# Kernel tuning notes

Measured on AMD Instinct MI355X. Metric: run time of the kernel, lower is better.

Reference implementation:

```python
import jax, jax.numpy as jnp
import numpy as np

B, L, C, D = 4, 128, 1024, 512

def setup_inputs() -> dict:
    key = jax.random.key(0)
    ks = jax.random.split(key, 6)
    scale = 1.0 / np.sqrt(D)
    return {
        "hidden": jax.random.normal(ks[0], (B, L, D), dtype=jnp.float32),
        "ctx": jax.random.normal(ks[1], (B, C, D), dtype=jnp.float32),
        "W": jax.random.normal(ks[2], (D, D), dtype=jnp.float32) * scale,
        "U": jax.random.normal(ks[3], (D, D), dtype=jnp.float32) * scale,
        "U_b": jax.random.normal(ks[4], (D,), dtype=jnp.float32) * scale,
        "V": jax.random.normal(ks[5], (D,), dtype=jnp.float32) * scale,
    }

def reference(hidden, ctx, W, U, U_b, V):
    # Bahdanau additive attention: softmax_j V . tanh(W h_i + U c_j + b)
    wq = jnp.einsum('bld,ed->ble', hidden, W)          # [B, L, D]
    uc = jnp.einsum('bcd,ed->bce', ctx, U) + U_b       # [B, C, D]
    s = jnp.tanh(wq[:, :, None, :] + uc[:, None, :, :])  # [B, L, C, D]
    align = jnp.einsum('blcd,d->blc', s, V)            # [B, L, C]
    return jax.nn.softmax(align, axis=-1)
```

## Files before the change

kernel.cpp:

```cpp
#include <hip/hip_runtime.h>
#include <hip/hip_bf16.h>


#define SCALE2 2.8853900817779268f
#define PART (4 * 128 * 1024)

typedef _Float16 f16x8 __attribute__((ext_vector_type(8)));
typedef float f32x4 __attribute__((ext_vector_type(4)));

__device__ __forceinline__ void gload16(const void* g, void* l) {
    __builtin_amdgcn_global_load_lds(
        (const __attribute__((address_space(1))) void*)g,
        (__attribute__((address_space(3))) void*)l,
        16, 0, 0);
}

__global__ __launch_bounds__(256) void gemm_mfma(
    const float* __restrict__ hidden, const float* __restrict__ ctx,
    const float* __restrict__ Wmat, const float* __restrict__ Umat,
    const float* __restrict__ U_b,
    float* __restrict__ ewq_t, float* __restrict__ euc_t)
{
    __shared__ __align__(16) _Float16 Xh[2][64][40];
    __shared__ __align__(16) _Float16 Xl[2][64][40];
    __shared__ __align__(16) _Float16 Wh[2][64][40];
    __shared__ __align__(16) _Float16 Wl[2][64][40];

    const int tid  = threadIdx.x;
    const int lane = tid & 63;
    const int w    = tid >> 6;

    const float *X, *Wm, *bias;
    float* Ct;
    int m0, crow0, Mb, bshift;
    {
        int gb = blockIdx.x;
        if (gb < 64) {
            m0 = (gb & 7) * 64; crow0 = (gb >> 3) * 64;
            X = hidden; Wm = Wmat; bias = nullptr; Ct = ewq_t; Mb = 128; bshift = 7;
        } else {
            int g = gb - 64;
            m0 = (g & 7) * 64; crow0 = (g >> 3) * 64;
            X = ctx; Wm = Umat; bias = U_b; Ct = euc_t; Mb = 1024; bshift = 10;
        }
    }

    const int sr = tid >> 2;
    const int sk = (tid & 3) * 8;
    const float* xsrc = X  + (size_t)(crow0 + sr) * 512 + sk;
    const float* wsrc = Wm + (size_t)(m0    + sr) * 512 + sk;

    f32x4 acc[4];
#pragma unroll
    for (int t = 0; t < 4; ++t) acc[t] = (f32x4){0.f, 0.f, 0.f, 0.f};

    float xr[8], wr[8];
    {
        float4 a = *(const float4*)(xsrc);
        float4 b = *(const float4*)(xsrc + 4);
        float4 c = *(const float4*)(wsrc);
        float4 d = *(const float4*)(wsrc + 4);
        xr[0]=a.x; xr[1]=a.y; xr[2]=a.z; xr[3]=a.w; xr[4]=b.x; xr[5]=b.y; xr[6]=b.z; xr[7]=b.w;
        wr[0]=c.x; wr[1]=c.y; wr[2]=c.z; wr[3]=c.w; wr[4]=d.x; wr[5]=d.y; wr[6]=d.z; wr[7]=d.w;
        f16x8 xh, xl, wh, wl;
#pragma unroll
        for (int i = 0; i < 8; ++i) {
            xh[i] = (_Float16)xr[i]; xl[i] = (_Float16)(xr[i] - (float)xh[i]);
            wh[i] = (_Float16)wr[i]; wl[i] = (_Float16)(wr[i] - (float)wh[i]);
        }
        *(f16x8*)&Xh[0][sr][sk] = xh; *(f16x8*)&Xl[0][sr][sk] = xl;
        *(f16x8*)&Wh[0][sr][sk] = wh; *(f16x8*)&Wl[0][sr][sk] = wl;
    }

    const int fr = lane & 15;
    const int fk = (lane >> 4) * 8;
    const int mrow = w * 16 + fr;

    for (int kc = 0; kc < 16; ++kc) {
        if (kc < 15) {
            float4 a = *(const float4*)(xsrc + (kc + 1) * 32);
            float4 b = *(const float4*)(xsrc + (kc + 1) * 32 + 4);
            float4 c = *(const float4*)(wsrc + (kc + 1) * 32);
            float4 d = *(const float4*)(wsrc + (kc + 1) * 32 + 4);
            xr[0]=a.x; xr[1]=a.y; xr[2]=a.z; xr[3]=a.w; xr[4]=b.x; xr[5]=b.y; xr[6]=b.z; xr[7]=b.w;
            wr[0]=c.x; wr[1]=c.y; wr[2]=c.z; wr[3]=c.w; wr[4]=d.x; wr[5]=d.y; wr[6]=d.z; wr[7]=d.w;
        }
        __syncthreads();
        const int bu = kc & 1;
        const f16x8 ah = *(const f16x8*)&Wh[bu][mrow][fk];
        const f16x8 al = *(const f16x8*)&Wl[bu][mrow][fk];
#pragma unroll
        for (int t = 0; t < 4; ++t) {
            const f16x8 bh = *(const f16x8*)&Xh[bu][t * 16 + fr][fk];
            const f16x8 bl = *(const f16x8*)&Xl[bu][t * 16 + fr][fk];
            acc[t] = __builtin_amdgcn_mfma_f32_16x16x32_f16(ah, bh, acc[t], 0, 0, 0);
            acc[t] = __builtin_amdgcn_mfma_f32_16x16x32_f16(ah, bl, acc[t], 0, 0, 0);
            acc[t] = __builtin_amdgcn_mfma_f32_16x16x32_f16(al, bh, acc[t], 0, 0, 0);
        }
        if (kc < 15) {
            f16x8 xh, xl, wh, wl;
#pragma unroll
            for (int i = 0; i < 8; ++i) {
                xh[i] = (_Float16)xr[i]; xl[i] = (_Float16)(xr[i] - (float)xh[i]);
                wh[i] = (_Float16)wr[i]; wl[i] = (_Float16)(wr[i] - (float)wh[i]);
            }
            *(f16x8*)&Xh[bu ^ 1][sr][sk] = xh; *(f16x8*)&Xl[bu ^ 1][sr][sk] = xl;
            *(f16x8*)&Wh[bu ^ 1][sr][sk] = wh; *(f16x8*)&Wl[bu ^ 1][sr][sk] = wl;
        }
    }

    const int rbase = m0 + w * 16 + (lane >> 4) * 4;
    float bl4[4] = {0.f, 0.f, 0.f, 0.f};
    if (bias) {
        float4 t = *(const float4*)&bias[rbase];
        bl4[0] = t.x; bl4[1] = t.y; bl4[2] = t.z; bl4[3] = t.w;
    }
    const int bidx = crow0 >> bshift;
    const int cl0  = crow0 & (Mb - 1);
    float* obase = Ct + ((size_t)bidx * 512 + rbase) * Mb + cl0 + fr;
#pragma unroll
    for (int r = 0; r < 4; ++r)
#pragma unroll
        for (int t = 0; t < 4; ++t)
            obase[(size_t)r * Mb + t * 16] =
                __builtin_amdgcn_exp2f(SCALE2 * (acc[t][r] + bl4[r]));
}

__global__ __launch_bounds__(256) void fused_align10(
    const float* __restrict__ ewq_t,
    const float* __restrict__ euc_t,
    const float* __restrict__ Vv,
    float* __restrict__ pout, float* __restrict__ pws)
{
    __shared__ __align__(16) float uc_s[2][16][256];
    __shared__ __align__(16) float wq_s[2][16][16];
    __shared__ float v_s[64];

    const int tid  = threadIdx.x;
    const int lane = tid & 63;
    const int w    = __builtin_amdgcn_readfirstlane(tid >> 6);
    const int c0   = blockIdx.x * 256;
    const int l0   = blockIdx.y * 16;
    const int z    = blockIdx.z;
    const int b    = z >> 3, h = z & 7;
    const int d0   = h * 64;

    const float* ucb = euc_t + ((size_t)b * 512 + d0) * 1024 + c0;
    const float* wqb = ewq_t + ((size_t)b * 512 + d0) * 128 + l0;

    if (tid < 64) v_s[tid] = Vv[d0 + tid];

#define STAGE(buf, chunk)                                                     \
    {                                                                         \
        _Pragma("unroll")                                                     \
        for (int i_ = 0; i_ < 4; ++i_) {                                      \
            const int d_ = w * 4 + i_;                                        \
            gload16(ucb + (size_t)((chunk) * 16 + d_) * 1024 + lane * 4,      \
                    &uc_s[buf][d_][0]);                                       \
        }                                                                     \
        if (w == 0)                                                           \
            gload16(wqb + (size_t)((chunk) * 16 + (lane >> 2)) * 128 +        \
                        (lane & 3) * 4,                                       \
                    &wq_s[buf][0][0]);                                        \
    }

    float acc[4][4];
#pragma unroll
    for (int i = 0; i < 4; ++i)
#pragma unroll
        for (int k = 0; k < 4; ++k) acc[i][k] = 0.0f;

#define COMPUTE(bu, ch)                                                       \
    do {                                                                      \
        float vr[16];                                                         \
        _Pragma("unroll")                                                     \
        for (int j_ = 0; j_ < 4; ++j_) {                                      \
            const float4 v4_ = *(const float4*)&v_s[(ch) * 16 + j_ * 4];      \
            vr[j_ * 4 + 0] = v4_.x; vr[j_ * 4 + 1] = v4_.y;                   \
            vr[j_ * 4 + 2] = v4_.z; vr[j_ * 4 + 3] = v4_.w;                   \
        }                                                                     \
        float nn[4][4], dn[4][4];                                             \
        {                                                                     \
            const float4 e = *(const float4*)&uc_s[bu][0][lane * 4];          \
            const float4 q = *(const float4*)&wq_s[bu][0][w * 4];             \
            const float ea[4] = {e.x, e.y, e.z, e.w};                         \
            const float qa[4] = {q.x, q.y, q.z, q.w};                         \
            _Pragma("unroll")                                                 \
            for (int i = 0; i < 4; ++i)                                       \
                _Pragma("unroll")                                             \
                for (int k = 0; k < 4; ++k) {                                 \
                    dn[i][k] = fmaf(qa[i], ea[k], 1.0f);                      \
                    nn[i][k] = vr[0];                                         \
                }                                                             \
        }                                                                     \
        _Pragma("unroll")                                                     \
        for (int dd = 1; dd < 16; ++dd) {                                     \
            const float4 e = *(const float4*)&uc_s[bu][dd][lane * 4];         \
            const float4 q = *(const float4*)&wq_s[bu][dd][w * 4];            \
            const float ea[4] = {e.x, e.y, e.z, e.w};                         \
            const float qa[4] = {q.x, q.y, q.z, q.w};                         \
            const float vv = vr[dd];                                          \
            _Pragma("unroll")                                                 \
            for (int i = 0; i < 4; ++i)                                       \
                _Pragma("unroll")                                             \
                for (int k = 0; k < 4; ++k) {                                 \
                    const float t_ = fmaf(qa[i], ea[k], 1.0f);                \
                    nn[i][k] = fmaf(nn[i][k], t_, vv * dn[i][k]);             \
                    dn[i][k] *= t_;                                           \
                }                                                             \
        }                                                                     \
        _Pragma("unroll")                                                     \
        for (int i = 0; i < 4; ++i)                                           \
            _Pragma("unroll")                                                 \
            for (int k = 0; k < 4; ++k)                                       \
                acc[i][k] = fmaf(nn[i][k],                                    \
                                 __builtin_amdgcn_rcpf(dn[i][k]), acc[i][k]); \
    } while (0)

    STAGE(0, 0);
    __syncthreads();

    for (int cc = 0; cc < 2; ++cc) {
        STAGE(1, 2 * cc + 1);
        COMPUTE(0, 2 * cc);
        __syncthreads();
        if (cc == 0) STAGE(0, 2);
        COMPUTE(1, 2 * cc + 1);
        __syncthreads();
    }
#undef STAGE
#undef COMPUTE

    float* pp = (h == 0) ? pout : pws + (size_t)(h - 1) * PART;
#pragma unroll
    for (int i = 0; i < 4; ++i) {
        float4 r;
        r.x = -2.0f * acc[i][0]; r.y = -2.0f * acc[i][1];
        r.z = -2.0f * acc[i][2]; r.w = -2.0f * acc[i][3];
        *(float4*)(pp + ((size_t)b * 128 + l0 + w * 4 + i) * 1024 + c0 + lane * 4) = r;
    }
}

__global__ __launch_bounds__(256) void softmax4(
    float* __restrict__ data, const float* __restrict__ pws)
{
    const int row  = blockIdx.x * 4 + (threadIdx.x >> 6);
    const int lane = threadIdx.x & 63;
    float* p = data + (size_t)row * 1024;

    float4 x[4];
#pragma unroll
    for (int j = 0; j < 4; ++j) x[j] = *(const float4*)(p + j * 256 + lane * 4);
#pragma unroll
    for (int t = 0; t < 7; ++t) {
        const float* q = pws + (size_t)t * PART + (size_t)row * 1024;
#pragma unroll
        for (int j = 0; j < 4; ++j) {
            const float4 a = *(const float4*)(q + j * 256 + lane * 4);
            x[j].x += a.x; x[j].y += a.y; x[j].z += a.z; x[j].w += a.w;
        }
    }

    float m = x[0].x;
#pragma unroll
    for (int j = 0; j < 4; ++j) {
        m = fmaxf(m, x[j].x); m = fmaxf(m, x[j].y);
        m = fmaxf(m, x[j].z); m = fmaxf(m, x[j].w);
    }
#pragma unroll
    for (int mask = 32; mask >= 1; mask >>= 1) m = fmaxf(m, __shfl_xor(m, mask, 64));

    const float LOG2E = 1.4426950408889634f;
    float s = 0.0f;
#pragma unroll
    for (int j = 0; j < 4; ++j) {
        x[j].x = __builtin_amdgcn_exp2f((x[j].x - m) * LOG2E);
        x[j].y = __builtin_amdgcn_exp2f((x[j].y - m) * LOG2E);
        x[j].z = __builtin_amdgcn_exp2f((x[j].z - m) * LOG2E);
        x[j].w = __builtin_amdgcn_exp2f((x[j].w - m) * LOG2E);
        s += x[j].x + x[j].y + x[j].z + x[j].w;
    }
#pragma unroll
    for (int mask = 32; mask >= 1; mask >>= 1) s += __shfl_xor(s, mask, 64);
    const float r = __builtin_amdgcn_rcpf(s);
#pragma unroll
    for (int j = 0; j < 4; ++j) {
        x[j].x *= r; x[j].y *= r; x[j].z *= r; x[j].w *= r;
        *(float4*)(p + j * 256 + lane * 4) = x[j];
    }
}

extern "C" void kernel_launch(void* const* d_in, const int* in_sizes, int n_in,
                              void* d_out, int out_size, void* d_ws, size_t ws_size,
                              hipStream_t stream)
{
    const float* hidden = (const float*)d_in[0];
    const float* ctx    = (const float*)d_in[1];
    const float* W      = (const float*)d_in[2];
    const float* U      = (const float*)d_in[3];
    const float* U_b    = (const float*)d_in[4];
    const float* V      = (const float*)d_in[5];
    float* out = (float*)d_out;

    float* ewq_t = (float*)d_ws;
    float* euc_t = ewq_t + 4 * 512 * 128;
    float* pws   = euc_t + 4 * 512 * 1024;

    gemm_mfma<<<576, 256, 0, stream>>>(hidden, ctx, W, U, U_b, ewq_t, euc_t);
    fused_align10<<<dim3(4, 8, 32), 256, 0, stream>>>(ewq_t, euc_t, V, out, pws);
    softmax4<<<128, 256, 0, stream>>>(out, pws);
}
```

Measured before the change: 51.81 us.

## Deepen GEMM prefetch, raise align priority, spread softmax one row per block

The GEMM kernel now keeps two register sets of raw fp32 data, so global loads are issued two K-chunks ahead and the loop is fully unrolled, which hides load latency better. The alignment kernel raises wave priority with s_setprio around its compute section to favour math issue over the staging waves. Softmax now uses one 256-thread block per row instead of one wave per row, giving 512 blocks for more parallelism, at the cost of LDS cross-wave reductions and two barriers. The deeper prefetch raises register pressure in the GEMM.

```diff
diff --git a/kernel.cpp b/kernel.cpp
--- a/kernel.cpp
+++ b/kernel.cpp
@@ -54,60 +54,74 @@
 #pragma unroll
     for (int t = 0; t < 4; ++t) acc[t] = (f32x4){0.f, 0.f, 0.f, 0.f};
 
-    float xr[8], wr[8];
-    {
-        float4 a = *(const float4*)(xsrc);
-        float4 b = *(const float4*)(xsrc + 4);
-        float4 c = *(const float4*)(wsrc);
-        float4 d = *(const float4*)(wsrc + 4);
-        xr[0]=a.x; xr[1]=a.y; xr[2]=a.z; xr[3]=a.w; xr[4]=b.x; xr[5]=b.y; xr[6]=b.z; xr[7]=b.w;
-        wr[0]=c.x; wr[1]=c.y; wr[2]=c.z; wr[3]=c.w; wr[4]=d.x; wr[5]=d.y; wr[6]=d.z; wr[7]=d.w;
-        f16x8 xh, xl, wh, wl;
-#pragma unroll
-        for (int i = 0; i < 8; ++i) {
-            xh[i] = (_Float16)xr[i]; xl[i] = (_Float16)(xr[i] - (float)xh[i]);
-            wh[i] = (_Float16)wr[i]; wl[i] = (_Float16)(wr[i] - (float)wh[i]);
-        }
-        *(f16x8*)&Xh[0][sr][sk] = xh; *(f16x8*)&Xl[0][sr][sk] = xl;
-        *(f16x8*)&Wh[0][sr][sk] = wh; *(f16x8*)&Wl[0][sr][sk] = wl;
+    float xrA[8], wrA[8], xrB[8], wrB[8];
+
+#define LOADRAW(xr_, wr_, chunk)                                              \
+    {                                                                         \
+        float4 a_ = *(const float4*)(xsrc + (chunk) * 32);                    \
+        float4 b_ = *(const float4*)(xsrc + (chunk) * 32 + 4);                \
+        float4 c_ = *(const float4*)(wsrc + (chunk) * 32);                    \
+        float4 d_ = *(const float4*)(wsrc + (chunk) * 32 + 4);                \
+        xr_[0]=a_.x; xr_[1]=a_.y; xr_[2]=a_.z; xr_[3]=a_.w;                   \
+        xr_[4]=b_.x; xr_[5]=b_.y; xr_[6]=b_.z; xr_[7]=b_.w;                   \
+        wr_[0]=c_.x; wr_[1]=c_.y; wr_[2]=c_.z; wr_[3]=c_.w;                   \
+        wr_[4]=d_.x; wr_[5]=d_.y; wr_[6]=d_.z; wr_[7]=d_.w;                   \
+    }
+
+#define CVTWRITE(xr_, wr_, buf)                                               \
+    {                                                                         \
+        f16x8 xh_, xl_, wh_, wl_;                                             \
+        _Pragma("unroll")                                                     \
+        for (int i_ = 0; i_ < 8; ++i_) {                                      \
+            xh_[i_] = (_Float16)xr_[i_];                                      \
+            xl_[i_] = (_Float16)(xr_[i_] - (float)xh_[i_]);                   \
+            wh_[i_] = (_Float16)wr_[i_];                                      \
+            wl_[i_] = (_Float16)(wr_[i_] - (float)wh_[i_]);                   \
+        }                                                                     \
+        *(f16x8*)&Xh[buf][sr][sk] = xh_; *(f16x8*)&Xl[buf][sr][sk] = xl_;     \
+        *(f16x8*)&Wh[buf][sr][sk] = wh_; *(f16x8*)&Wl[buf][sr][sk] = wl_;     \
     }
 
     const int fr = lane & 15;
     const int fk = (lane >> 4) * 8;
     const int mrow = w * 16 + fr;
 
-    for (int kc = 0; kc < 16; ++kc) {
-        if (kc < 15) {
-            float4 a = *(const float4*)(xsrc + (kc + 1) * 32);
-            float4 b = *(const float4*)(xsrc + (kc + 1) * 32 + 4);
-            float4 c = *(const float4*)(wsrc + (kc + 1) * 32);
-            float4 d = *(const float4*)(wsrc + (kc + 1) * 32 + 4);
-            xr[0]=a.x; xr[1]=a.y; xr[2]=a.z; xr[3]=a.w; xr[4]=b.x; xr[5]=b.y; xr[6]=b.z; xr[7]=b.w;
-            wr[0]=c.x; wr[1]=c.y; wr[2]=c.z; wr[3]=c.w; wr[4]=d.x; wr[5]=d.y; wr[6]=d.z; wr[7]=d.w;
-        }
-        __syncthreads();
-        const int bu = kc & 1;
-        const f16x8 ah = *(const f16x8*)&Wh[bu][mrow][fk];
-        const f16x8 al = *(const f16x8*)&Wl[bu][mrow][fk];
-#pragma unroll
-        for (int t = 0; t < 4; ++t) {
-            const f16x8 bh = *(const f16x8*)&Xh[bu][t * 16 + fr][fk];
-            const f16x8 bl = *(const f16x8*)&Xl[bu][t * 16 + fr][fk];
-            acc[t] = __builtin_amdgcn_mfma_f32_16x16x32_f16(ah, bh, acc[t], 0, 0, 0);
-            acc[t] = __builtin_amdgcn_mfma_f32_16x16x32_f16(ah, bl, acc[t], 0, 0, 0);
-            acc[t] = __builtin_amdgcn_mfma_f32_16x16x32_f16(al, bh, acc[t], 0, 0, 0);
-        }
-        if (kc < 15) {
-            f16x8 xh, xl, wh, wl;
-#pragma unroll
-            for (int i = 0; i < 8; ++i) {
-                xh[i] = (_Float16)xr[i]; xl[i] = (_Float16)(xr[i] - (float)xh[i]);
-                wh[i] = (_Float16)wr[i]; wl[i] = (_Float16)(wr[i] - (float)wh[i]);
-            }
-            *(f16x8*)&Xh[bu ^ 1][sr][sk] = xh; *(f16x8*)&Xl[bu ^ 1][sr][sk] = xl;
-            *(f16x8*)&Wh[bu ^ 1][sr][sk] = wh; *(f16x8*)&Wl[bu ^ 1][sr][sk] = wl;
-        }
-    }
+#define MFMA_CHUNK(bu)                                                        \
+    {                                                                         \
+        const f16x8 ah = *(const f16x8*)&Wh[bu][mrow][fk];                    \
+        const f16x8 al = *(const f16x8*)&Wl[bu][mrow][fk];                    \
+        _Pragma("unroll")                                                     \
+        for (int t = 0; t < 4; ++t) {                                         \
+            const f16x8 bh = *(const f16x8*)&Xh[bu][t * 16 + fr][fk];         \
+            const f16x8 bl = *(const f16x8*)&Xl[bu][t * 16 + fr][fk];         \
+            acc[t] = __builtin_amdgcn_mfma_f32_16x16x32_f16(ah, bh, acc[t], 0, 0, 0); \
+            acc[t] = __builtin_amdgcn_mfma_f32_16x16x32_f16(ah, bl, acc[t], 0, 0, 0); \
+            acc[t] = __builtin_amdgcn_mfma_f32_16x16x32_f16(al, bh, acc[t], 0, 0, 0); \
+        }                                                                     \
+    }
+
+    LOADRAW(xrA, wrA, 0);
+    CVTWRITE(xrA, wrA, 0);
+    LOADRAW(xrA, wrA, 1);
+    __syncthreads();
+
+#define ITER(kc, xP, wP, xQ, wQ)                                              \
+    {                                                                         \
+        if ((kc) + 2 < 16) LOADRAW(xQ, wQ, (kc) + 2);                         \
+        MFMA_CHUNK((kc) & 1);                                                 \
+        if ((kc) + 1 < 16) CVTWRITE(xP, wP, ((kc) + 1) & 1);                  \
+        __syncthreads();                                                      \
+    }
+
+#pragma unroll
+    for (int kc2 = 0; kc2 < 16; kc2 += 2) {
+        ITER(kc2,     xrA, wrA, xrB, wrB);
+        ITER(kc2 + 1, xrB, wrB, xrA, wrA);
+    }
+#undef ITER
+#undef MFMA_CHUNK
+#undef CVTWRITE
+#undef LOADRAW
 
     const int rbase = m0 + w * 16 + (lane >> 4) * 4;
     float bl4[4] = {0.f, 0.f, 0.f, 0.f};
@@ -126,7 +140,7 @@
                 __builtin_amdgcn_exp2f(SCALE2 * (acc[t][r] + bl4[r]));
 }
 
-__global__ __launch_bounds__(256) void fused_align10(
+__global__ __launch_bounds__(256) void fused_align11(
     const float* __restrict__ ewq_t,
     const float* __restrict__ euc_t,
     const float* __restrict__ Vv,
@@ -172,6 +186,7 @@
 
 #define COMPUTE(bu, ch)                                                       \
     do {                                                                      \
+        __builtin_amdgcn_s_setprio(1);                                        \
         float vr[16];                                                         \
         _Pragma("unroll")                                                     \
         for (int j_ = 0; j_ < 4; ++j_) {                                      \
@@ -215,6 +230,7 @@
             for (int k = 0; k < 4; ++k)                                       \
                 acc[i][k] = fmaf(nn[i][k],                                    \
                                  __builtin_amdgcn_rcpf(dn[i][k]), acc[i][k]); \
+        __builtin_amdgcn_s_setprio(0);                                        \
     } while (0)
 
     STAGE(0, 0);
@@ -241,53 +257,46 @@
     }
 }
 
-__global__ __launch_bounds__(256) void softmax4(
+__global__ __launch_bounds__(256) void softmax5(
     float* __restrict__ data, const float* __restrict__ pws)
 {
-    const int row  = blockIdx.x * 4 + (threadIdx.x >> 6);
-    const int lane = threadIdx.x & 63;
+    __shared__ float red[8];
+    const int row  = blockIdx.x;
+    const int tid  = threadIdx.x;
+    const int w    = tid >> 6;
+    const int lane = tid & 63;
     float* p = data + (size_t)row * 1024;
 
-    float4 x[4];
-#pragma unroll
-    for (int j = 0; j < 4; ++j) x[j] = *(const float4*)(p + j * 256 + lane * 4);
+    float4 x = *(const float4*)(p + tid * 4);
 #pragma unroll
     for (int t = 0; t < 7; ++t) {
-        const float* q = pws + (size_t)t * PART + (size_t)row * 1024;
-#pragma unroll
-        for (int j = 0; j < 4; ++j) {
-            const float4 a = *(const float4*)(q + j * 256 + lane * 4);
-            x[j].x += a.x; x[j].y += a.y; x[j].z += a.z; x[j].w += a.w;
-        }
-    }
-
-    float m = x[0].x;
-#pragma unroll
-    for (int j = 0; j < 4; ++j) {
-        m = fmaxf(m, x[j].x); m = fmaxf(m, x[j].y);
-        m = fmaxf(m, x[j].z); m = fmaxf(m, x[j].w);
-    }
+        const float4 a =
+            *(const float4*)(pws + (size_t)t * PART + (size_t)row * 1024 + tid * 4);
+        x.x += a.x; x.y += a.y; x.z += a.z; x.w += a.w;
+    }
+
+    float m = fmaxf(fmaxf(x.x, x.y), fmaxf(x.z, x.w));
 #pragma unroll
     for (int mask = 32; mask >= 1; mask >>= 1) m = fmaxf(m, __shfl_xor(m, mask, 64));
+    if (lane == 0) red[w] = m;
+    __syncthreads();
+    m = fmaxf(fmaxf(red[0], red[1]), fmaxf(red[2], red[3]));
 
     const float LOG2E = 1.4426950408889634f;
-    float s = 0.0f;
-#pragma unroll
-    for (int j = 0; j < 4; ++j) {
-        x[j].x = __builtin_amdgcn_exp2f((x[j].x - m) * LOG2E);
-        x[j].y = __builtin_amdgcn_exp2f((x[j].y - m) * LOG2E);
-        x[j].z = __builtin_amdgcn_exp2f((x[j].z - m) * LOG2E);
-        x[j].w = __builtin_amdgcn_exp2f((x[j].w - m) * LOG2E);
-        s += x[j].x + x[j].y + x[j].z + x[j].w;
-    }
+    x.x = __builtin_amdgcn_exp2f((x.x - m) * LOG2E);
+    x.y = __builtin_amdgcn_exp2f((x.y - m) * LOG2E);
+    x.z = __builtin_amdgcn_exp2f((x.z - m) * LOG2E);
+    x.w = __builtin_amdgcn_exp2f((x.w - m) * LOG2E);
+    float s = (x.x + x.y) + (x.z + x.w);
 #pragma unroll
     for (int mask = 32; mask >= 1; mask >>= 1) s += __shfl_xor(s, mask, 64);
+    if (lane == 0) red[4 + w] = s;
+    __syncthreads();
+    s = (red[4] + red[5]) + (red[6] + red[7]);
+
     const float r = __builtin_amdgcn_rcpf(s);
-#pragma unroll
-    for (int j = 0; j < 4; ++j) {
-        x[j].x *= r; x[j].y *= r; x[j].z *= r; x[j].w *= r;
-        *(float4*)(p + j * 256 + lane * 4) = x[j];
-    }
+    x.x *= r; x.y *= r; x.z *= r; x.w *= r;
+    *(float4*)(p + tid * 4) = x;
 }
 
 extern "C" void kernel_launch(void* const* d_in, const int* in_sizes, int n_in,
@@ -307,6 +316,6 @@
     float* pws   = euc_t + 4 * 512 * 1024;
 
     gemm_mfma<<<576, 256, 0, stream>>>(hidden, ctx, W, U, U_b, ewq_t, euc_t);
-    fused_align10<<<dim3(4, 8, 32), 256, 0, stream>>>(ewq_t, euc_t, V, out, pws);
-    softmax4<<<128, 256, 0, stream>>>(out, pws);
-}
+    fused_align11<<<dim3(4, 8, 32), 256, 0, stream>>>(ewq_t, euc_t, V, out, pws);
+    softmax5<<<512, 256, 0, stream>>>(out, pws);
+}
```

New measurement: 52.87 us. 2.1% more time.
